# Performance work log

Hardware: AMD Instinct MI355X
Metric: run time of the kernel (lower is better)

The kernel has to match this reference:

```python
import jax, jax.numpy as jnp
import numpy as np

L, B, T, C, H, V, CTX = 4, 2, 1024, 1024, 16, 50257, 2048
D = C // H
EPS = 1e-5
NEG_SLOPE = 0.01


def layer_norm(x, w, b):
    mu = jnp.mean(x, axis=-1, keepdims=True)
    var = jnp.mean(jnp.square(x - mu), axis=-1, keepdims=True)
    return (x - mu) * jax.lax.rsqrt(var + EPS) * w + b


def setup_inputs() -> dict:
    key = jax.random.key(0)
    ks = jax.random.split(key, 8)
    s = 0.02  # init std as in _init_weights
    return {
        "idx": jax.random.randint(ks[0], (B, T), 0, V),
        "wte": jax.random.normal(ks[1], (V, C), jnp.float32) * s,
        "wpe": jax.random.normal(ks[2], (CTX, C), jnp.float32) * s,
        "ln1_w": jnp.ones((L, C), jnp.float32),
        "ln1_b": jnp.zeros((L, C), jnp.float32),
        "attn_w": jax.random.normal(ks[3], (L, C, 3 * C), jnp.float32) * s,
        "attn_b": jnp.zeros((L, 3 * C), jnp.float32),
        "proj_w": jax.random.normal(ks[4], (L, C, C), jnp.float32) * s,
        "proj_b": jnp.zeros((L, C), jnp.float32),
        "ln2_w": jnp.ones((L, C), jnp.float32),
        "ln2_b": jnp.zeros((L, C), jnp.float32),
        "fc_w": jax.random.normal(ks[5], (L, C, 4 * C), jnp.float32) * s,
        "fc_b": jnp.zeros((L, 4 * C), jnp.float32),
        "fcproj_w": jax.random.normal(ks[6], (L, 4 * C, C), jnp.float32) * s,
        "fcproj_b": jnp.zeros((L, C), jnp.float32),
        "lnf_w": jnp.ones((C,), jnp.float32),
        "lnf_b": jnp.zeros((C,), jnp.float32),
    }


def reference(idx, wte, wpe, ln1_w, ln1_b, attn_w, attn_b, proj_w, proj_b,
              ln2_w, ln2_b, fc_w, fc_b, fcproj_w, fcproj_b, lnf_w, lnf_b):
    t = idx.shape[1]
    x = wte[idx] + wpe[:t]  # [B,T,C]; dropout=0 => identity
    causal = jnp.tril(jnp.ones((t, t), bool))  # [T,T]
    scale = 1.0 / np.sqrt(D)
    for l in range(L):
        # --- causal self-attention ---
        h = layer_norm(x, ln1_w[l], ln1_b[l])
        qkv = h @ attn_w[l] + attn_b[l]  # [B,T,3C]
        q, k, v = jnp.split(qkv, 3, axis=-1)
        q = q.reshape(B, t, H, D)
        k = k.reshape(B, t, H, D)
        v = v.reshape(B, t, H, D)
        att = jnp.einsum('bthd,bshd->bhts', q, k) * scale  # [B,H,T,T]
        att = jnp.where(causal, att, -jnp.inf)
        att = jax.nn.softmax(att, axis=-1)
        y = jnp.einsum('bhts,bshd->bthd', att, v).reshape(B, t, C)
        x = x + y @ proj_w[l] + proj_b[l]
        # --- MLP ---
        h = layer_norm(x, ln2_w[l], ln2_b[l])
        h = h @ fc_w[l] + fc_b[l]
        h = jnp.where(h >= 0, h, NEG_SLOPE * h)  # LeakyReLU(0.01)
        x = x + h @ fcproj_w[l] + fcproj_b[l]
    x = layer_norm(x, lnf_w, lnf_b)
    # targets=None path: lm_head on last position only, tied weight = wte
    logits = x[:, -1:, :] @ wte.T  # [B,1,V]
    return logits
```

## Files before the change

### kernel.cpp

```cpp
#include <hip/hip_runtime.h>
#include <hip/hip_bf16.h>


#define TT 1024
#define CC 1024
#define NHEAD 16
#define DHEAD 64
#define NBATCH 2
#define VOCAB 50257

typedef __attribute__((ext_vector_type(8))) short bf16x8;
typedef __attribute__((ext_vector_type(4))) float f32x4;
typedef __attribute__((ext_vector_type(16))) float f32x16;

#define GPTR(p) (const __attribute__((address_space(1))) void*)(p)
#define LPTR(p) (__attribute__((address_space(3))) void*)(p)

__device__ __forceinline__ unsigned short f2bf(float f) {
  union { float f; unsigned u; } v; v.f = f;
  unsigned r = v.u + 0x7fffu + ((v.u >> 16) & 1u);
  return (unsigned short)(r >> 16);
}
__device__ __forceinline__ float bf2f(unsigned short u) {
  union { unsigned u; float f; } v; v.u = ((unsigned)u) << 16;
  return v.f;
}

__device__ __forceinline__ f32x4 mfma_bf16(bf16x8 a, bf16x8 b, f32x4 c) {
  return __builtin_amdgcn_mfma_f32_16x16x32_bf16(a, b, c, 0, 0, 0);
}
__device__ __forceinline__ f32x16 mfma32_bf16(bf16x8 a, bf16x8 b, f32x16 c) {
  return __builtin_amdgcn_mfma_f32_32x32x16_bf16(a, b, c, 0, 0, 0);
}

__device__ __forceinline__ unsigned pk2(float lo, float hi) {
  return (unsigned)f2bf(lo) | ((unsigned)f2bf(hi) << 16);
}

__global__ __launch_bounds__(256) void embedln_k(const int* __restrict__ idx,
    const float* __restrict__ wte, const float* __restrict__ wpe,
    const float* __restrict__ lw, const float* __restrict__ lb,
    float* __restrict__ x, unsigned short* __restrict__ h)
{
  __shared__ float rs[4], rss[4];
  const int row = blockIdx.x;
  const int t = row & (TT - 1);
  const int tok = idx[row];
  const int tid = threadIdx.x, wave = tid >> 6, lane = tid & 63;
  float4 va = ((const float4*)(wte + (size_t)tok * CC))[tid];
  float4 vp = ((const float4*)(wpe + (size_t)t * CC))[tid];
  float4 v = make_float4(va.x + vp.x, va.y + vp.y, va.z + vp.z, va.w + vp.w);
  ((float4*)(x + (size_t)row * CC))[tid] = v;
  float s  = v.x + v.y + v.z + v.w;
  float ss = v.x*v.x + v.y*v.y + v.z*v.z + v.w*v.w;
#pragma unroll
  for (int off = 1; off < 64; off <<= 1) {
    s  += __shfl_xor(s, off, 64);
    ss += __shfl_xor(ss, off, 64);
  }
  if (lane == 0) { rs[wave] = s; rss[wave] = ss; }
  __syncthreads();
  s  = rs[0] + rs[1] + rs[2] + rs[3];
  ss = rss[0] + rss[1] + rss[2] + rss[3];
  float mu = s * (1.f / CC);
  float var = ss * (1.f / CC) - mu * mu;
  float rstd = rsqrtf(var + 1e-5f);
  float4 wv = ((const float4*)lw)[tid];
  float4 bv = ((const float4*)lb)[tid];
  float o0 = (v.x - mu) * rstd * wv.x + bv.x;
  float o1 = (v.y - mu) * rstd * wv.y + bv.y;
  float o2 = (v.z - mu) * rstd * wv.z + bv.z;
  float o3 = (v.w - mu) * rstd * wv.w + bv.w;
  ((uint2*)(h + (size_t)row * CC))[tid] = make_uint2(pk2(o0, o1), pk2(o2, o3));
}

__global__ __launch_bounds__(256) void redln_k(float* __restrict__ x,
    const unsigned short* __restrict__ P, const float* __restrict__ bias,
    const float* __restrict__ lw, const float* __restrict__ lb,
    unsigned short* __restrict__ out, int splits)
{
  int row = blockIdx.x * 4 + (threadIdx.x >> 6);
  int lane = threadIdx.x & 63;
  const int c0 = lane * 16;
  float* xw = x + (size_t)row * CC + c0;
  float4 v[4];
#pragma unroll
  for (int i = 0; i < 4; ++i) v[i] = *(const float4*)(xw + i * 4);
  {
    const float4* b4 = (const float4*)(bias + c0);
#pragma unroll
    for (int i = 0; i < 4; ++i) {
      float4 bv = b4[i];
      v[i].x += bv.x; v[i].y += bv.y; v[i].z += bv.z; v[i].w += bv.w;
    }
  }
  for (int sp = 0; sp < splits; ++sp) {
    const unsigned short* pp = P + ((size_t)sp * 2048 + row) * CC + c0;
    bf16x8 pa = *(const bf16x8*)pp;
    bf16x8 pb = *(const bf16x8*)(pp + 8);
    v[0].x += bf2f((unsigned short)pa[0]); v[0].y += bf2f((unsigned short)pa[1]);
    v[0].z += bf2f((unsigned short)pa[2]); v[0].w += bf2f((unsigned short)pa[3]);
    v[1].x += bf2f((unsigned short)pa[4]); v[1].y += bf2f((unsigned short)pa[5]);
    v[1].z += bf2f((unsigned short)pa[6]); v[1].w += bf2f((unsigned short)pa[7]);
    v[2].x += bf2f((unsigned short)pb[0]); v[2].y += bf2f((unsigned short)pb[1]);
    v[2].z += bf2f((unsigned short)pb[2]); v[2].w += bf2f((unsigned short)pb[3]);
    v[3].x += bf2f((unsigned short)pb[4]); v[3].y += bf2f((unsigned short)pb[5]);
    v[3].z += bf2f((unsigned short)pb[6]); v[3].w += bf2f((unsigned short)pb[7]);
  }
  float s = 0.f, ss = 0.f;
#pragma unroll
  for (int i = 0; i < 4; ++i) {
    *(float4*)(xw + i * 4) = v[i];
    s  += v[i].x + v[i].y + v[i].z + v[i].w;
    ss += v[i].x*v[i].x + v[i].y*v[i].y + v[i].z*v[i].z + v[i].w*v[i].w;
  }
#pragma unroll
  for (int off = 1; off < 64; off <<= 1) {
    s  += __shfl_xor(s, off, 64);
    ss += __shfl_xor(ss, off, 64);
  }
  float mu = s * (1.f / CC);
  float var = ss * (1.f / CC) - mu * mu;
  float rstd = rsqrtf(var + 1e-5f);
  const float* wr = lw + c0;
  const float* br = lb + c0;
  unsigned q[8];
#pragma unroll
  for (int i = 0; i < 4; ++i) {
    float4 wv = *(const float4*)(wr + i * 4);
    float4 bv = *(const float4*)(br + i * 4);
    float o0 = (v[i].x - mu) * rstd * wv.x + bv.x;
    float o1 = (v[i].y - mu) * rstd * wv.y + bv.y;
    float o2 = (v[i].z - mu) * rstd * wv.z + bv.z;
    float o3 = (v[i].w - mu) * rstd * wv.w + bv.w;
    q[i*2+0] = pk2(o0, o1);
    q[i*2+1] = pk2(o2, o3);
  }
  uint4* op = (uint4*)(out + (size_t)row * CC + c0);
  op[0] = make_uint4(q[0], q[1], q[2], q[3]);
  op[1] = make_uint4(q[4], q[5], q[6], q[7]);
}

__global__ __launch_bounds__(256) void wconv_all_k(
    const float* __restrict__ attn_w, unsigned short* __restrict__ wt_attn,
    const float* __restrict__ proj_w, unsigned short* __restrict__ wt_proj,
    const float* __restrict__ fc_w,   unsigned short* __restrict__ wt_fc,
    const float* __restrict__ fcp_w,  unsigned short* __restrict__ wt_fcp)
{
  int b = blockIdx.x;
  const float* W; unsigned short* Wt; int K, N, kx, ny;
  if (b < 3072) {
    int layer = b / 768, tI = b % 768;
    K = 1024; N = 3072;
    W = attn_w + (size_t)layer * K * N; Wt = wt_attn + (size_t)layer * K * N;
    kx = tI % 16; ny = tI / 16;
  } else if (b < 3840) {
    b -= 3072; int layer = b / 256, tI = b % 256;
    K = 1024; N = 1024;
    W = proj_w + (size_t)layer * K * N; Wt = wt_proj + (size_t)layer * K * N;
    kx = tI % 16; ny = tI / 16;
  } else if (b < 6912) {
    b -= 3840; int layer = b / 1024, tI = b % 1024;
    K = 1024; N = 4096;
    W = fc_w + (size_t)layer * K * N; Wt = wt_fc + (size_t)layer * K * N;
    kx = tI % 16; ny = tI / 16;
  } else {
    b -= 6912; int layer = b / 1024, tI = b % 1024;
    K = 4096; N = 1024;
    W = fcp_w + (size_t)layer * K * N; Wt = wt_fcp + (size_t)layer * K * N;
    kx = tI % 64; ny = tI / 64;
  }
  __shared__ float tile[64][65];
  const int k0 = kx << 6, n0 = ny << 6;
  const int t = threadIdx.x;
  {
    const int r = t >> 4, c4 = t & 15;
#pragma unroll
    for (int p = 0; p < 4; ++p) {
      int kr = r + (p << 4);
      float4 v = *(const float4*)(W + (size_t)(k0 + kr) * N + n0 + (c4 << 2));
      tile[kr][(c4 << 2) + 0] = v.x;
      tile[kr][(c4 << 2) + 1] = v.y;
      tile[kr][(c4 << 2) + 2] = v.z;
      tile[kr][(c4 << 2) + 3] = v.w;
    }
  }
  __syncthreads();
  {
    const int n = t >> 2, kq = t & 3;
    bf16x8 o0, o1;
#pragma unroll
    for (int e = 0; e < 8; ++e) o0[e] = (short)f2bf(tile[(kq << 4) + e][n]);
#pragma unroll
    for (int e = 0; e < 8; ++e) o1[e] = (short)f2bf(tile[(kq << 4) + 8 + e][n]);
    unsigned short* dst = Wt + (size_t)(n0 + n) * K + k0 + (kq << 4);
    *(bf16x8*)dst = o0;
    *(bf16x8*)(dst + 8) = o1;
  }
}

#define MODE_QKV  0
#define MODE_PART 1
#define MODE_FC   2

template<int MODE>
__global__ __launch_bounds__(256) void gemm_k(
    const unsigned short* __restrict__ A,
    const unsigned short* __restrict__ Wt,
    const float* __restrict__ bias,
    unsigned short* __restrict__ obf,
    unsigned short* __restrict__ q_o,
    unsigned short* __restrict__ k_o,
    unsigned short* __restrict__ v_o,
    int M, int N, int K, int kchunk, int ncol0)
{
  __shared__ alignas(16) unsigned short Asm[2][128 * 64];
  __shared__ alignas(16) unsigned short Bsm[2][128 * 64];
  const int tid  = threadIdx.x;
  const int wave = tid >> 6, lane = tid & 63;
  const int rl = lane & 31, hi = lane >> 5;
  const int nTM = M >> 7, nTN = N >> 7;
  int bid = blockIdx.x;
  const int mt = bid % nTM; bid /= nTM;
  const int nt = bid % nTN;
  const int s  = bid / nTN;
  const int m0 = mt << 7, n0 = nt << 7;
  const int kb = s * kchunk;
  const int nIter = kchunk >> 6;
  const int wm = (wave >> 1) << 6, wn = (wave & 1) << 6;
  f32x16 acc[2][2] = {};

#define STAGE(BUF, K0)                                                        \
  {                                                                           \
    _Pragma("unroll")                                                         \
    for (int c = 0; c < 4; ++c) {                                             \
      const int seg = (wave << 2) + c;                                        \
      const int g = (seg << 6) + lane;                                        \
      const int row = g >> 3, kq = g & 7;                                     \
      const int kqs = kq ^ (row & 7);                                         \
      const unsigned short* asrc = A  + (size_t)(m0 + row) * K + (K0) + (kqs << 3); \
      const unsigned short* bsrc = Wt + (size_t)(n0 + row) * K + (K0) + (kqs << 3); \
      __builtin_amdgcn_global_load_lds(GPTR(asrc), LPTR(&Asm[BUF][seg << 9]), 16, 0, 0); \
      __builtin_amdgcn_global_load_lds(GPTR(bsrc), LPTR(&Bsm[BUF][seg << 9]), 16, 0, 0); \
    }                                                                         \
  }

  STAGE(0, kb);
  if (nIter > 1) STAGE(1, kb + 64);

  for (int t = 0; t < nIter; ++t) {
    const int cur = t & 1;
    if (t + 1 < nIter) { asm volatile("s_waitcnt vmcnt(8)" ::: "memory"); }
    else               { asm volatile("s_waitcnt vmcnt(0)" ::: "memory"); }
    __builtin_amdgcn_sched_barrier(0);
    __builtin_amdgcn_s_barrier();

    const unsigned short* As = &Asm[cur][0];
    const unsigned short* Bs = &Bsm[cur][0];
#pragma unroll
    for (int sl = 0; sl < 4; ++sl) {
      const int c = sl * 2 + hi;
      const int cs = (c ^ (rl & 7)) << 3;
      bf16x8 a0 = *(const bf16x8*)(As + ((wm + rl) << 6) + cs);
      bf16x8 a1 = *(const bf16x8*)(As + ((wm + 32 + rl) << 6) + cs);
      bf16x8 b0 = *(const bf16x8*)(Bs + ((wn + rl) << 6) + cs);
      bf16x8 b1 = *(const bf16x8*)(Bs + ((wn + 32 + rl) << 6) + cs);
      acc[0][0] = mfma32_bf16(a0, b0, acc[0][0]);
      acc[0][1] = mfma32_bf16(a0, b1, acc[0][1]);
      acc[1][0] = mfma32_bf16(a1, b0, acc[1][0]);
      acc[1][1] = mfma32_bf16(a1, b1, acc[1][1]);
    }
    __builtin_amdgcn_sched_barrier(0);
    __builtin_amdgcn_s_barrier();
    if (t + 2 < nIter) STAGE(cur, kb + ((t + 2) << 6));
  }
#undef STAGE

#pragma unroll
  for (int j = 0; j < 2; ++j) {
    int gc = n0 + wn + j * 32 + rl;
    int gcol = ncol0 + gc;
    float bv = (MODE == MODE_PART) ? 0.f : bias[gcol];
#pragma unroll
    for (int i = 0; i < 2; ++i) {
      int gr0 = m0 + wm + i * 32 + 4 * hi;
#pragma unroll
      for (int reg = 0; reg < 16; ++reg) {
        int grow = gr0 + (reg & 3) + 8 * (reg >> 2);
        float val = acc[i][j][reg] + bv;
        if (MODE == MODE_QKV) {
          int which = gcol >> 10;
          int head = (gcol >> 6) & 15;
          int d = gcol & 63;
          int bb = grow >> 10, tt2 = grow & (TT - 1);
          size_t bhb = ((size_t)((bb << 4) + head)) << 16;
          if (which == 2)      v_o[bhb + ((size_t)d << 10) + tt2] = f2bf(val);
          else if (which == 1) k_o[bhb + ((size_t)tt2 << 6) + d] = f2bf(val);
          else                 q_o[bhb + ((size_t)tt2 << 6) + d] = f2bf(val);
        } else if (MODE == MODE_FC) {
          val = (val >= 0.f) ? val : 0.01f * val;
          obf[(size_t)grow * N + gc] = f2bf(val);
        } else {
          obf[((size_t)s * M + grow) * N + gc] = f2bf(val);
        }
      }
    }
  }
}

__global__ __launch_bounds__(256) void attn_k(
    const unsigned short* __restrict__ Qb,
    const unsigned short* __restrict__ Kb,
    const unsigned short* __restrict__ Vb,
    unsigned short* __restrict__ ybuf)
{
  __shared__ alignas(16) unsigned short Ksm[64][72];
  __shared__ alignas(16) unsigned short Vtsm[64][64];
  __shared__ alignas(16) unsigned short Psm[4][16][72];
  const int tid = threadIdx.x;
  const int wave = tid >> 6, lane = tid & 63;
  const int lg = lane >> 4, ll = lane & 15;
  const int qt = blockIdx.x & 15, bh = blockIdx.x >> 4;
  const int b = bh >> 4, h = bh & 15;
  const size_t base = (size_t)bh << 16;
  const int q0 = qt << 6;
  const float SC = 0.125f * 1.44269504f;

  const int qrow = q0 + wave * 16 + ll;
  bf16x8 aq0 = *(const bf16x8*)(Qb + base + ((size_t)qrow << 6) + (lg << 3));
  bf16x8 aq1 = *(const bf16x8*)(Qb + base + ((size_t)qrow << 6) + 32 + (lg << 3));

  f32x4 accy[4] = {};
  float m_run[4], l_run[4];
#pragma unroll
  for (int r = 0; r < 4; ++r) { m_run[r] = -1e30f; l_run[r] = 0.f; }

  const int sk_row = tid >> 3, sk_cq = tid & 7;
  const int sv_d = tid & 63, sv_kq = tid >> 6;
  const int qg0 = q0 + wave * 16 + (lg << 2);

  for (int kb = 0; kb <= qt; ++kb) {
    const int kbase = kb << 6;
#pragma unroll
    for (int p = 0; p < 2; ++p) {
      int r = sk_row + (p << 5);
      bf16x8 kv = *(const bf16x8*)(Kb + base + ((size_t)(kbase + r) << 6) + (sk_cq << 3));
      *(bf16x8*)&Ksm[r][sk_cq << 3] = kv;
    }
#pragma unroll
    for (int p = 0; p < 2; ++p) {
      int kq8 = sv_kq + (p << 2);
      bf16x8 wv = *(const bf16x8*)(Vb + base + ((size_t)sv_d << 10) + kbase + (kq8 << 3));
      int u = kq8 ^ (sv_d & 7);
      *(bf16x8*)&Vtsm[sv_d][u << 3] = wv;
    }
    __syncthreads();

    float p_[4][4];
    float rmax[4] = {-1e30f, -1e30f, -1e30f, -1e30f};
#pragma unroll
    for (int kk = 0; kk < 4; ++kk) {
      f32x4 z = {};
      bf16x8 bk0 = *(const bf16x8*)&Ksm[kk * 16 + ll][lg << 3];
      bf16x8 bk1 = *(const bf16x8*)&Ksm[kk * 16 + ll][32 + (lg << 3)];
      z = mfma_bf16(aq0, bk0, z);
      z = mfma_bf16(aq1, bk1, z);
      int key = kbase + kk * 16 + ll;
#pragma unroll
      for (int r = 0; r < 4; ++r) {
        float v = z[r] * SC;
        v = (key > qg0 + r) ? -1e30f : v;
        p_[kk][r] = v;
        rmax[r] = fmaxf(rmax[r], v);
      }
    }
#pragma unroll
    for (int off = 1; off < 16; off <<= 1)
#pragma unroll
      for (int r = 0; r < 4; ++r)
        rmax[r] = fmaxf(rmax[r], __shfl_xor(rmax[r], off, 64));

    float alpha[4], rsum[4];
#pragma unroll
    for (int r = 0; r < 4; ++r) {
      float mn = fmaxf(m_run[r], rmax[r]);
      alpha[r] = exp2f(m_run[r] - mn);
      m_run[r] = mn;
      rsum[r] = 0.f;
    }
#pragma unroll
    for (int kk = 0; kk < 4; ++kk)
#pragma unroll
      for (int r = 0; r < 4; ++r) {
        float e = exp2f(p_[kk][r] - m_run[r]);
        p_[kk][r] = e;
        rsum[r] += e;
      }
#pragma unroll
    for (int off = 1; off < 16; off <<= 1)
#pragma unroll
      for (int r = 0; r < 4; ++r)
        rsum[r] += __shfl_xor(rsum[r], off, 64);
#pragma unroll
    for (int r = 0; r < 4; ++r)
      l_run[r] = l_run[r] * alpha[r] + rsum[r];
#pragma unroll
    for (int df = 0; df < 4; ++df)
#pragma unroll
      for (int r = 0; r < 4; ++r)
        accy[df][r] *= alpha[r];

#pragma unroll
    for (int kk = 0; kk < 4; ++kk)
#pragma unroll
      for (int r = 0; r < 4; ++r)
        Psm[wave][(lg << 2) + r][kk * 16 + ll] = f2bf(p_[kk][r]);
    bf16x8 pa0 = *(const bf16x8*)&Psm[wave][ll][lg << 3];
    bf16x8 pa1 = *(const bf16x8*)&Psm[wave][ll][32 + (lg << 3)];

#pragma unroll
    for (int df = 0; df < 4; ++df) {
      int d = df * 16 + ll;
      int u0 = lg ^ (d & 7);
      int u1 = (4 + lg) ^ (d & 7);
      bf16x8 bv0 = *(const bf16x8*)&Vtsm[d][u0 << 3];
      bf16x8 bv1 = *(const bf16x8*)&Vtsm[d][u1 << 3];
      accy[df] = mfma_bf16(pa0, bv0, accy[df]);
      accy[df] = mfma_bf16(pa1, bv1, accy[df]);
    }
    __syncthreads();
  }

#pragma unroll
  for (int df = 0; df < 4; ++df)
#pragma unroll
    for (int r = 0; r < 4; ++r) {
      int qr = qg0 + r;
      float y = accy[df][r] / l_run[r];
      ybuf[(((size_t)((b << 10) + qr)) << 10) + (h << 6) + df * 16 + ll] = f2bf(y);
    }
}


__global__ __launch_bounds__(256) void qlast_k(
    const unsigned short* __restrict__ hbuf,
    const float* __restrict__ Wq,
    float* __restrict__ qpart)
{
  __shared__ float xs[2][128];
  const int tid = threadIdx.x, ks = blockIdx.y;
  {
    const int b = tid >> 7, j = tid & 127;
    xs[b][j] = bf2f(hbuf[((size_t)(b * TT + TT - 1)) * CC + ks * 128 + j]);
  }
  __syncthreads();
  const int n = blockIdx.x * 256 + tid;
  float a0 = 0.f, a1 = 0.f;
  const float* wp = Wq + (size_t)(ks * 128) * 3072 + n;
  for (int k = 0; k < 128; k += 8)
#pragma unroll
    for (int u = 0; u < 8; ++u) {
      float w = wp[(size_t)(k + u) * 3072];
      a0 += xs[0][k + u] * w;
      a1 += xs[1][k + u] * w;
    }
  qpart[(size_t)(ks * 2 + 0) * 1024 + n] = a0;
  qpart[(size_t)(ks * 2 + 1) * 1024 + n] = a1;
}

__global__ __launch_bounds__(256) void attnlast2_k(
    const float* __restrict__ qpart, const float* __restrict__ bq,
    const unsigned short* __restrict__ Kb,
    const unsigned short* __restrict__ Vb,
    float* __restrict__ y_last)
{
  __shared__ float qs[64];
  __shared__ float wm[4], wl[4], wacc[4][64];
  const int tid = threadIdx.x;
  const int wave = tid >> 6, lane = tid & 63;
  const int bh = blockIdx.x;
  const int b = bh >> 4, h = bh & 15;
  const size_t base = (size_t)bh << 16;
  if (tid < 64) {
    const int col = h * 64 + tid;
    float q = bq[col];
#pragma unroll
    for (int ks = 0; ks < 8; ++ks)
      q += qpart[(size_t)(ks * 2 + b) * 1024 + col];
    qs[tid] = q;
  }
  __syncthreads();

  float m_w = -1e30f, l_w = 0.f, acc = 0.f;
  for (int ks = 0; ks < 4; ++ks) {
    const int key = ks * 256 + wave * 64 + lane;
    float s = 0.f;
    const unsigned short* kp = Kb + base + ((size_t)key << 6);
#pragma unroll
    for (int o = 0; o < 8; ++o) {
      bf16x8 kv = *(const bf16x8*)(kp + (o << 3));
#pragma unroll
      for (int e = 0; e < 8; ++e)
        s += qs[(o << 3) + e] * bf2f((unsigned short)kv[e]);
    }
    s *= 0.125f;
    float m = s;
#pragma unroll
    for (int off = 1; off < 64; off <<= 1)
      m = fmaxf(m, __shfl_xor(m, off, 64));
    float mn = fmaxf(m_w, m);
    float alpha = __expf(m_w - mn);
    m_w = mn;
    float p = __expf(s - mn);
    float ps = p;
#pragma unroll
    for (int off = 1; off < 64; off <<= 1)
      ps += __shfl_xor(ps, off, 64);
    l_w = l_w * alpha + ps;
    float a2 = 0.f;
    const unsigned short* vp = Vb + base + ((size_t)lane << 10) + ks * 256 + wave * 64;
#pragma unroll
    for (int j8 = 0; j8 < 8; ++j8) {
      bf16x8 vv = *(const bf16x8*)(vp + (j8 << 3));
#pragma unroll
      for (int e = 0; e < 8; ++e) {
        float pj = __shfl(p, (j8 << 3) + e, 64);
        a2 += pj * bf2f((unsigned short)vv[e]);
      }
    }
    acc = acc * alpha + a2;
  }
  if (lane == 0) { wm[wave] = m_w; wl[wave] = l_w; }
  wacc[wave][lane] = acc;
  __syncthreads();
  if (wave == 0) {
    float m0 = fmaxf(fmaxf(wm[0], wm[1]), fmaxf(wm[2], wm[3]));
    float lt = 0.f, at = 0.f;
#pragma unroll
    for (int sI = 0; sI < 4; ++sI) {
      float f = __expf(wm[sI] - m0);
      lt += wl[sI] * f;
      at += wacc[sI][lane] * f;
    }
    y_last[b * CC + h * 64 + lane] = at / lt;
  }
}

__global__ __launch_bounds__(256) void projpart_k(
    const float* __restrict__ ylast,
    const float* __restrict__ W,
    float* __restrict__ ppart)
{
  __shared__ float xs[2][128];
  const int tid = threadIdx.x, ks = blockIdx.y;
  {
    const int b = tid >> 7, j = tid & 127;
    xs[b][j] = ylast[b * 1024 + ks * 128 + j];
  }
  __syncthreads();
  const int n = blockIdx.x * 256 + tid;
  float a0 = 0.f, a1 = 0.f;
  const float* wp = W + (size_t)(ks * 128) * 1024 + n;
  for (int k = 0; k < 128; k += 8)
#pragma unroll
    for (int u = 0; u < 8; ++u) {
      float w = wp[(size_t)(k + u) * 1024];
      a0 += xs[0][k + u] * w;
      a1 += xs[1][k + u] * w;
    }
  ppart[(size_t)(ks * 2 + 0) * 1024 + n] = a0;
  ppart[(size_t)(ks * 2 + 1) * 1024 + n] = a1;
}

__global__ __launch_bounds__(256) void fclast_k(
    const float* __restrict__ x, const float* __restrict__ ppart,
    const float* __restrict__ pbias,
    const float* __restrict__ lw, const float* __restrict__ lb,
    const float* __restrict__ W,
    float* __restrict__ fcpart)
{
  __shared__ float xs[2][1024];
  const int tid = threadIdx.x;
  const int wave = tid >> 6, lane = tid & 63;
  if (wave < 2) {
    const int c0 = lane * 16;
    const float* xr = x + ((size_t)(wave * TT + TT - 1)) * CC + c0;
    float4 v[4];
    float s = 0.f, ss = 0.f;
#pragma unroll
    for (int i = 0; i < 4; ++i) {
      v[i] = *(const float4*)(xr + i * 4);
      float4 bv = *(const float4*)(pbias + c0 + i * 4);
      v[i].x += bv.x; v[i].y += bv.y; v[i].z += bv.z; v[i].w += bv.w;
    }
#pragma unroll
    for (int sp = 0; sp < 8; ++sp) {
      const float* pp = ppart + (size_t)(sp * 2 + wave) * 1024 + c0;
#pragma unroll
      for (int i = 0; i < 4; ++i) {
        float4 pv = *(const float4*)(pp + i * 4);
        v[i].x += pv.x; v[i].y += pv.y; v[i].z += pv.z; v[i].w += pv.w;
      }
    }
#pragma unroll
    for (int i = 0; i < 4; ++i) {
      s  += v[i].x + v[i].y + v[i].z + v[i].w;
      ss += v[i].x*v[i].x + v[i].y*v[i].y + v[i].z*v[i].z + v[i].w*v[i].w;
    }
#pragma unroll
    for (int off = 1; off < 64; off <<= 1) {
      s  += __shfl_xor(s, off, 64);
      ss += __shfl_xor(ss, off, 64);
    }
    float mu = s * (1.f / CC);
    float var = ss * (1.f / CC) - mu * mu;
    float rstd = rsqrtf(var + 1e-5f);
#pragma unroll
    for (int i = 0; i < 4; ++i) {
      float4 wv = *(const float4*)(lw + c0 + i * 4);
      float4 bv = *(const float4*)(lb + c0 + i * 4);
      xs[wave][c0 + i * 4 + 0] = (v[i].x - mu) * rstd * wv.x + bv.x;
      xs[wave][c0 + i * 4 + 1] = (v[i].y - mu) * rstd * wv.y + bv.y;
      xs[wave][c0 + i * 4 + 2] = (v[i].z - mu) * rstd * wv.z + bv.z;
      xs[wave][c0 + i * 4 + 3] = (v[i].w - mu) * rstd * wv.w + bv.w;
    }
  }
  __syncthreads();
  const int ks = blockIdx.y;
  const int n = blockIdx.x * 256 + tid;
  float a0 = 0.f, a1 = 0.f;
  const float* wp = W + (size_t)(ks * 128) * 4096 + n;
  for (int k = 0; k < 128; k += 8)
#pragma unroll
    for (int u = 0; u < 8; ++u) {
      float w = wp[(size_t)(k + u) * 4096];
      a0 += xs[0][ks * 128 + k + u] * w;
      a1 += xs[1][ks * 128 + k + u] * w;
    }
  fcpart[(size_t)(ks * 2 + 0) * 4096 + n] = a0;
  fcpart[(size_t)(ks * 2 + 1) * 4096 + n] = a1;
}

__global__ __launch_bounds__(256) void fcprojpart_k(
    const float* __restrict__ fcpart, const float* __restrict__ fcbias,
    const float* __restrict__ W,
    float* __restrict__ fppart)
{
  __shared__ float hs[2][512];
  const int tid = threadIdx.x, ks = blockIdx.y;
#pragma unroll
  for (int i = 0; i < 4; ++i) {
    const int e = tid + 256 * i;
    const int b = e >> 9, j = e & 511;
    const int c = ks * 512 + j;
    float v = fcbias[c];
#pragma unroll
    for (int sp = 0; sp < 8; ++sp)
      v += fcpart[(size_t)(sp * 2 + b) * 4096 + c];
    hs[b][j] = (v >= 0.f) ? v : 0.01f * v;
  }
  __syncthreads();
  const int n = blockIdx.x * 256 + tid;
  float a0 = 0.f, a1 = 0.f;
  const float* wp = W + (size_t)(ks * 512) * 1024 + n;
  for (int k = 0; k < 512; k += 8)
#pragma unroll
    for (int u = 0; u < 8; ++u) {
      float w = wp[(size_t)(k + u) * 1024];
      a0 += hs[0][k + u] * w;
      a1 += hs[1][k + u] * w;
    }
  fppart[(size_t)(ks * 2 + 0) * 1024 + n] = a0;
  fppart[(size_t)(ks * 2 + 1) * 1024 + n] = a1;
}

__global__ __launch_bounds__(256) void lnfmerge_k(const float* __restrict__ x,
    const float* __restrict__ ppart, const float* __restrict__ pbias,
    const float* __restrict__ fppart, const float* __restrict__ fpbias,
    const float* __restrict__ lw, const float* __restrict__ lb,
    float* __restrict__ xf)
{
  __shared__ float rs[4], rss[4];
  const int row = blockIdx.x;
  const int tid = threadIdx.x;
  const int wave = tid >> 6, lane = tid & 63;
  const int c0 = tid * 4;
  float4 v = *(const float4*)(x + ((size_t)(row * TT + TT - 1)) * CC + c0);
  {
    float4 b1 = *(const float4*)(pbias + c0);
    float4 b2 = *(const float4*)(fpbias + c0);
    v.x += b1.x + b2.x; v.y += b1.y + b2.y;
    v.z += b1.z + b2.z; v.w += b1.w + b2.w;
  }
#pragma unroll
  for (int sp = 0; sp < 8; ++sp) {
    float4 a = *(const float4*)(ppart + (size_t)(sp * 2 + row) * 1024 + c0);
    float4 b = *(const float4*)(fppart + (size_t)(sp * 2 + row) * 1024 + c0);
    v.x += a.x + b.x; v.y += a.y + b.y;
    v.z += a.z + b.z; v.w += a.w + b.w;
  }
  float s  = v.x + v.y + v.z + v.w;
  float ss = v.x*v.x + v.y*v.y + v.z*v.z + v.w*v.w;
#pragma unroll
  for (int off = 1; off < 64; off <<= 1) {
    s  += __shfl_xor(s, off, 64);
    ss += __shfl_xor(ss, off, 64);
  }
  if (lane == 0) { rs[wave] = s; rss[wave] = ss; }
  __syncthreads();
  s  = rs[0] + rs[1] + rs[2] + rs[3];
  ss = rss[0] + rss[1] + rss[2] + rss[3];
  float mu = s * (1.f / CC);
  float var = ss * (1.f / CC) - mu * mu;
  float rstd = rsqrtf(var + 1e-5f);
  float4 wv = *(const float4*)(lw + c0);
  float4 bv = *(const float4*)(lb + c0);
  float4 o;
  o.x = (v.x - mu) * rstd * wv.x + bv.x;
  o.y = (v.y - mu) * rstd * wv.y + bv.y;
  o.z = (v.z - mu) * rstd * wv.z + bv.z;
  o.w = (v.w - mu) * rstd * wv.w + bv.w;
  *(float4*)(xf + (size_t)row * CC + c0) = o;
}

__global__ __launch_bounds__(256) void head_k(const float* __restrict__ xf,
    const float* __restrict__ wte, float* __restrict__ out)
{
  int v = (blockIdx.x << 2) + (threadIdx.x >> 6);
  if (v >= VOCAB) return;
  int lane = threadIdx.x & 63;
  const float4* wr = (const float4*)(wte + (size_t)v * CC);
  const float4* x0 = (const float4*)xf;
  const float4* x1 = (const float4*)(xf + CC);
  float a0 = 0.f, a1 = 0.f;
#pragma unroll
  for (int i = 0; i < 4; ++i) {
    float4 wv = wr[lane + i * 64];
    float4 p0 = x0[lane + i * 64];
    float4 p1 = x1[lane + i * 64];
    a0 += wv.x * p0.x + wv.y * p0.y + wv.z * p0.z + wv.w * p0.w;
    a1 += wv.x * p1.x + wv.y * p1.y + wv.z * p1.z + wv.w * p1.w;
  }
#pragma unroll
  for (int off = 1; off < 64; off <<= 1) {
    a0 += __shfl_xor(a0, off, 64);
    a1 += __shfl_xor(a1, off, 64);
  }
  if (lane == 0) {
    out[v] = a0;
    out[VOCAB + v] = a1;
  }
}

extern "C" void kernel_launch(void* const* d_in, const int* in_sizes, int n_in,
                              void* d_out, int out_size, void* d_ws, size_t ws_size,
                              hipStream_t stream)
{
  const int*   idx      = (const int*)d_in[0];
  const float* wte      = (const float*)d_in[1];
  const float* wpe      = (const float*)d_in[2];
  const float* ln1_w    = (const float*)d_in[3];
  const float* ln1_b    = (const float*)d_in[4];
  const float* attn_w   = (const float*)d_in[5];
  const float* attn_b   = (const float*)d_in[6];
  const float* proj_w   = (const float*)d_in[7];
  const float* proj_b   = (const float*)d_in[8];
  const float* ln2_w    = (const float*)d_in[9];
  const float* ln2_b    = (const float*)d_in[10];
  const float* fc_w     = (const float*)d_in[11];
  const float* fc_b     = (const float*)d_in[12];
  const float* fcproj_w = (const float*)d_in[13];
  const float* fcproj_b = (const float*)d_in[14];
  const float* lnf_w    = (const float*)d_in[15];
  const float* lnf_b    = (const float*)d_in[16];
  float* out = (float*)d_out;

  const size_t MB = 1u << 20;
  char* ws = (char*)d_ws;
  float*          x   = (float*)ws;
  unsigned short* h   = (unsigned short*)(ws + 8*MB);
  unsigned short* qb  = (unsigned short*)(ws + 12*MB);
  unsigned short* kb_ = (unsigned short*)(ws + 16*MB);
  unsigned short* vb  = (unsigned short*)(ws + 20*MB);
  unsigned short* yb  = (unsigned short*)(ws + 24*MB);
  unsigned short* hf  = (unsigned short*)(ws + 28*MB);
  char* sm = ws + 44*MB;
  float* xf     = (float*)(sm + 0);
  float* ylast  = (float*)(sm + 16*1024);
  float* qpart  = (float*)(sm + 64*1024);
  float* ppart  = (float*)(sm + 128*1024);
  float* fppart = (float*)(sm + 192*1024);
  float* fcpart = (float*)(sm + 256*1024);
  unsigned short* wt_attn   = (unsigned short*)(ws + 46*MB);
  unsigned short* wt_proj   = (unsigned short*)(ws + 70*MB);
  unsigned short* wt_fc     = (unsigned short*)(ws + 76*MB);
  unsigned short* wt_fcproj = (unsigned short*)(ws + 100*MB);
  unsigned short* Ppart     = (unsigned short*)(ws + 124*MB);

  embedln_k<<<NBATCH * TT, 256, 0, stream>>>(idx, wte, wpe, ln1_w, ln1_b, x, h);

  wconv_all_k<<<9984, 256, 0, stream>>>(attn_w, wt_attn, proj_w, wt_proj,
                                        fc_w, wt_fc, fcproj_w, wt_fcproj);

  for (int l = 0; l < 3; ++l) {
    gemm_k<MODE_QKV><<<16 * 24, 256, 0, stream>>>(h,
        wt_attn + (size_t)l * 3072 * 1024, attn_b + (size_t)l * 3 * CC,
        nullptr, qb, kb_, vb, 2048, 3072, 1024, 1024, 0);
    attn_k<<<NBATCH * NHEAD * 16, 256, 0, stream>>>(qb, kb_, vb, yb);
    gemm_k<MODE_PART><<<16 * 8 * 4, 256, 0, stream>>>(yb,
        wt_proj + (size_t)l * 1024 * 1024, nullptr,
        Ppart, nullptr, nullptr, nullptr, 2048, 1024, 1024, 256, 0);
    redln_k<<<512, 256, 0, stream>>>(x, Ppart, proj_b + l * CC,
        ln2_w + l * CC, ln2_b + l * CC, h, 4);
    gemm_k<MODE_FC><<<16 * 32, 256, 0, stream>>>(h,
        wt_fc + (size_t)l * 1024 * 4096, fc_b + (size_t)l * 4 * CC,
        hf, nullptr, nullptr, nullptr, 2048, 4096, 1024, 1024, 0);
    gemm_k<MODE_PART><<<16 * 8 * 4, 256, 0, stream>>>(hf,
        wt_fcproj + (size_t)l * 4096 * 1024, nullptr,
        Ppart, nullptr, nullptr, nullptr, 2048, 1024, 4096, 1024, 0);
    redln_k<<<512, 256, 0, stream>>>(x, Ppart, fcproj_b + l * CC,
        ln1_w + (l + 1) * CC, ln1_b + (l + 1) * CC, h, 4);
  }

  {
    const int l = 3;
    gemm_k<MODE_QKV><<<16 * 16, 256, 0, stream>>>(h,
        wt_attn + (size_t)l * 3072 * 1024 + (size_t)1024 * 1024,
        attn_b + (size_t)l * 3 * CC,
        nullptr, qb, kb_, vb, 2048, 2048, 1024, 1024, 1024);
    qlast_k<<<dim3(4, 8), 256, 0, stream>>>(h,
        attn_w + (size_t)l * CC * 3 * CC, qpart);
    attnlast2_k<<<32, 256, 0, stream>>>(qpart, attn_b + (size_t)l * 3 * CC,
        kb_, vb, ylast);
    projpart_k<<<dim3(4, 8), 256, 0, stream>>>(ylast,
        proj_w + (size_t)l * CC * CC, ppart);
    fclast_k<<<dim3(16, 8), 256, 0, stream>>>(x, ppart, proj_b + l * CC,
        ln2_w + l * CC, ln2_b + l * CC,
        fc_w + (size_t)l * CC * 4 * CC, fcpart);
    fcprojpart_k<<<dim3(4, 8), 256, 0, stream>>>(fcpart,
        fc_b + (size_t)l * 4 * CC, fcproj_w + (size_t)l * 4 * CC * CC, fppart);
    lnfmerge_k<<<2, 256, 0, stream>>>(x, ppart, proj_b + l * CC,
        fppart, fcproj_b + l * CC, lnf_w, lnf_b, xf);
  }

  head_k<<<(VOCAB + 3) / 4, 256, 0, stream>>>(xf, wte, out);
}
```

Measured before the change: 648.7 us.

## Single-buffer GEMM LDS for higher occupancy; raise MFMA priority in attention

The GEMM kernel drops its double-buffered LDS pipeline in favour of one buffer loaded and synchronised each K step. It also asks for four blocks per SM through launch bounds, so more waves can hide latency in place of explicit prefetch. Separately, the attention kernel raises wave priority around its MFMA sections with s_setprio. The risk is that global loads are no longer overlapped with compute inside a block, and that the register cap may cause spills.

```diff
diff --git a/kernel.cpp b/kernel.cpp
--- a/kernel.cpp
+++ b/kernel.cpp
@@ -204,7 +204,7 @@
 #define MODE_FC   2
 
 template<int MODE>
-__global__ __launch_bounds__(256) void gemm_k(
+__global__ __launch_bounds__(256, 4) void gemm_k(
     const unsigned short* __restrict__ A,
     const unsigned short* __restrict__ Wt,
     const float* __restrict__ bias,
@@ -214,8 +214,8 @@
     unsigned short* __restrict__ v_o,
     int M, int N, int K, int kchunk, int ncol0)
 {
-  __shared__ alignas(16) unsigned short Asm[2][128 * 64];
-  __shared__ alignas(16) unsigned short Bsm[2][128 * 64];
+  __shared__ alignas(16) unsigned short Asm[128 * 64];
+  __shared__ alignas(16) unsigned short Bsm[128 * 64];
   const int tid  = threadIdx.x;
   const int wave = tid >> 6, lane = tid & 63;
   const int rl = lane & 31, hi = lane >> 5;
@@ -230,7 +230,7 @@
   const int wm = (wave >> 1) << 6, wn = (wave & 1) << 6;
   f32x16 acc[2][2] = {};
 
-#define STAGE(BUF, K0)                                                        \
+#define STAGE(K0)                                                             \
   {                                                                           \
     _Pragma("unroll")                                                         \
     for (int c = 0; c < 4; ++c) {                                             \
@@ -240,39 +240,28 @@
       const int kqs = kq ^ (row & 7);                                         \
       const unsigned short* asrc = A  + (size_t)(m0 + row) * K + (K0) + (kqs << 3); \
       const unsigned short* bsrc = Wt + (size_t)(n0 + row) * K + (K0) + (kqs << 3); \
-      __builtin_amdgcn_global_load_lds(GPTR(asrc), LPTR(&Asm[BUF][seg << 9]), 16, 0, 0); \
-      __builtin_amdgcn_global_load_lds(GPTR(bsrc), LPTR(&Bsm[BUF][seg << 9]), 16, 0, 0); \
+      __builtin_amdgcn_global_load_lds(GPTR(asrc), LPTR(&Asm[seg << 9]), 16, 0, 0); \
+      __builtin_amdgcn_global_load_lds(GPTR(bsrc), LPTR(&Bsm[seg << 9]), 16, 0, 0); \
     }                                                                         \
   }
 
-  STAGE(0, kb);
-  if (nIter > 1) STAGE(1, kb + 64);
-
   for (int t = 0; t < nIter; ++t) {
-    const int cur = t & 1;
-    if (t + 1 < nIter) { asm volatile("s_waitcnt vmcnt(8)" ::: "memory"); }
-    else               { asm volatile("s_waitcnt vmcnt(0)" ::: "memory"); }
-    __builtin_amdgcn_sched_barrier(0);
-    __builtin_amdgcn_s_barrier();
-
-    const unsigned short* As = &Asm[cur][0];
-    const unsigned short* Bs = &Bsm[cur][0];
+    STAGE(kb + (t << 6));
+    __syncthreads();
 #pragma unroll
     for (int sl = 0; sl < 4; ++sl) {
       const int c = sl * 2 + hi;
       const int cs = (c ^ (rl & 7)) << 3;
-      bf16x8 a0 = *(const bf16x8*)(As + ((wm + rl) << 6) + cs);
-      bf16x8 a1 = *(const bf16x8*)(As + ((wm + 32 + rl) << 6) + cs);
-      bf16x8 b0 = *(const bf16x8*)(Bs + ((wn + rl) << 6) + cs);
-      bf16x8 b1 = *(const bf16x8*)(Bs + ((wn + 32 + rl) << 6) + cs);
+      bf16x8 a0 = *(const bf16x8*)(Asm + ((wm + rl) << 6) + cs);
+      bf16x8 a1 = *(const bf16x8*)(Asm + ((wm + 32 + rl) << 6) + cs);
+      bf16x8 b0 = *(const bf16x8*)(Bsm + ((wn + rl) << 6) + cs);
+      bf16x8 b1 = *(const bf16x8*)(Bsm + ((wn + 32 + rl) << 6) + cs);
       acc[0][0] = mfma32_bf16(a0, b0, acc[0][0]);
       acc[0][1] = mfma32_bf16(a0, b1, acc[0][1]);
       acc[1][0] = mfma32_bf16(a1, b0, acc[1][0]);
       acc[1][1] = mfma32_bf16(a1, b1, acc[1][1]);
     }
-    __builtin_amdgcn_sched_barrier(0);
-    __builtin_amdgcn_s_barrier();
-    if (t + 2 < nIter) STAGE(cur, kb + ((t + 2) << 6));
+    __syncthreads();
   }
 #undef STAGE
 
@@ -358,6 +347,7 @@
 
     float p_[4][4];
     float rmax[4] = {-1e30f, -1e30f, -1e30f, -1e30f};
+    __builtin_amdgcn_s_setprio(1);
 #pragma unroll
     for (int kk = 0; kk < 4; ++kk) {
       f32x4 z = {};
@@ -374,6 +364,7 @@
         rmax[r] = fmaxf(rmax[r], v);
       }
     }
+    __builtin_amdgcn_s_setprio(0);
 #pragma unroll
     for (int off = 1; off < 16; off <<= 1)
 #pragma unroll
@@ -418,6 +409,7 @@
     bf16x8 pa0 = *(const bf16x8*)&Psm[wave][ll][lg << 3];
     bf16x8 pa1 = *(const bf16x8*)&Psm[wave][ll][32 + (lg << 3)];
 
+    __builtin_amdgcn_s_setprio(1);
 #pragma unroll
     for (int df = 0; df < 4; ++df) {
       int d = df * 16 + ll;
@@ -428,6 +420,7 @@
       accy[df] = mfma_bf16(pa0, bv0, accy[df]);
       accy[df] = mfma_bf16(pa1, bv1, accy[df]);
     }
+    __builtin_amdgcn_s_setprio(0);
     __syncthreads();
   }
 
```

New measurement: 644.9 us (median of 4 runs). No clear change (-0.6%).
